# Optimization experiments

Hardware: AMD Instinct MI355X
Metric: run time of the kernel (lower is better)

Reference implementation:

```python
import jax, jax.numpy as jnp
import numpy as np

N = 100000     # total points
PBS = 500      # point_batch_size (hard-coded in module)
K = 100        # num_neighbors
KP = 15        # num_kernel_points
EPS = 1e-5


def _bn(x, g, b, axes):
    # torch BatchNorm in training mode: batch stats, biased variance
    m = jnp.mean(x, axis=axes, keepdims=True)
    v = jnp.var(x, axis=axes, keepdims=True)
    return (x - m) / jnp.sqrt(v + EPS) * g + b


def setup_inputs() -> dict:
    key = jax.random.key(0)
    ks = jax.random.split(key, 16)
    rn = lambda k, sh, s=1.0: jax.random.normal(k, sh, jnp.float32) * s
    return {
        "pts": rn(ks[0], (N, 3)),
        "normal": rn(ks[1], (N, 3)),
        "kp_points": rn(ks[2], (KP, 3)),
        "kp_weights": rn(ks[3], (KP, 3, 128), 0.3),
        "kp_sigma": jnp.float32(1.0),
        "conv1_w": rn(ks[4], (1024, 128), 128 ** -0.5),
        "conv1_b": rn(ks[5], (1024,), 0.02),
        "bn1_g": jnp.ones((1024,), jnp.float32),
        "bn1_b": jnp.zeros((1024,), jnp.float32),
        "fc1_w": rn(ks[6], (512, 1024), 1024 ** -0.5),
        "fc1_b": rn(ks[7], (512,), 0.02),
        "bn4_g": jnp.ones((512,), jnp.float32),
        "bn4_b": jnp.zeros((512,), jnp.float32),
        "fc2_w": rn(ks[8], (256, 512), 512 ** -0.5),
        "fc2_b": rn(ks[9], (256,), 0.02),
        "bn5_g": jnp.ones((256,), jnp.float32),
        "bn5_b": jnp.zeros((256,), jnp.float32),
        "fc3_w": rn(ks[10], (3, 256), 256 ** -0.5),
        "fc3_b": rn(ks[11], (3,), 0.02),
        "index": jax.random.randint(ks[12], (PBS,), 0, N, jnp.int32),
    }


def reference(pts, normal, kp_points, kp_weights, kp_sigma,
              conv1_w, conv1_b, bn1_g, bn1_b,
              fc1_w, fc1_b, bn4_g, bn4_b,
              fc2_w, fc2_b, bn5_g, bn5_b,
              fc3_w, fc3_b, index):
    sel = pts[index]                                               # [B,3]
    # L-inf pairwise distance and kNN (topk of -dist, as in the torch code)
    dist = jnp.max(jnp.abs(sel[:, None, :] - pts[None, :, :]), axis=-1)  # [B,N]
    _, nbr = jax.lax.top_k(-dist, K)                               # [B,K]
    rel = pts[nbr] - sel[:, None, :]                               # [B,K,3]

    # KPConv: gaussian weights vs kernel points, per-kernel-point linear map
    d2 = jnp.sum((rel[:, :, None, :] - kp_points[None, None]) ** 2, axis=-1)  # [B,K,KP]
    w = jnp.exp(-0.5 * d2 / (kp_sigma ** 2))
    wf = rel[:, :, None, :] * w[..., None]                         # [B,K,KP,3]
    h = jax.nn.relu(jnp.einsum('bnkc,kco->bno', wf, kp_weights))   # [B,K,128]

    # 1x1 conv 128->1024, relu then BN over (batch, points) per channel
    h = jnp.einsum('bnc,oc->bno', h, conv1_w) + conv1_b            # [B,K,1024]
    h = _bn(jax.nn.relu(h), bn1_g, bn1_b, (0, 1))
    feat = jnp.max(h, axis=1)                                      # [B,1024]

    feat = _bn(jax.nn.relu(feat @ fc1_w.T + fc1_b), bn4_g, bn4_b, (0,))
    feat = _bn(jax.nn.relu(feat @ fc2_w.T + fc2_b), bn5_g, bn5_b, (0,))
    feat = feat @ fc3_w.T + fc3_b                                  # [B,3]
    return feat, normal[index]
```

## Files before the change

### kernel.cpp

```cpp
#include <hip/hip_runtime.h>
#include <hip/hip_fp16.h>

#define NPTS 100000
#define NB 500
#define KNN 100
#define KPN 15
#define C1 128
#define C2 1024
#define C3 512
#define C4 256

typedef _Float16 half8 __attribute__((ext_vector_type(8)));
typedef float f32x4 __attribute__((ext_vector_type(4)));

__global__ __launch_bounds__(256) void gather_kernel(
    const float* __restrict__ pts, const float* __restrict__ normal,
    const int* __restrict__ index, float* __restrict__ sel,
    float* __restrict__ out2) {
  int b = blockIdx.x * 256 + threadIdx.x;
  if (b >= NB) return;
  int i = index[b];
  sel[b * 3 + 0] = pts[3 * i + 0];
  sel[b * 3 + 1] = pts[3 * i + 1];
  sel[b * 3 + 2] = pts[3 * i + 2];
  out2[b * 3 + 0] = normal[3 * i + 0];
  out2[b * 3 + 1] = normal[3 * i + 1];
  out2[b * 3 + 2] = normal[3 * i + 2];
}

#define KT 1024

__device__ __forceinline__ unsigned linf_bits(float px, float py, float pz,
                                              float sx, float sy, float sz) {
  float dx = fabsf(px - sx), dy = fabsf(py - sy), dz = fabsf(pz - sz);
  return __float_as_uint(fmaxf(fmaxf(dx, dy), dz));
}

__global__ __launch_bounds__(KT) void knn_kernel(
    const float* __restrict__ pts, const float* __restrict__ sel,
    int* __restrict__ nbr) {
  const int b = blockIdx.x;
  const int tid = threadIdx.x;
  __shared__ unsigned hist[4096];
  __shared__ unsigned chunksum[256];
  __shared__ unsigned s_prefix;
  __shared__ int s_kneed, s_base, s_cnt, s_direct, s_cnt2;
  __shared__ unsigned cand_bits[1024];
  __shared__ int cand_idx[1024];

  const float sx = sel[b * 3 + 0], sy = sel[b * 3 + 1], sz = sel[b * 3 + 2];
  const float4* base4 = (const float4*)pts;

  for (int j = tid; j < 4096; j += KT) hist[j] = 0;
  __syncthreads();
  {
    float4 c[6], n[6];
    int i0 = tid * 8;
#pragma unroll
    for (int j = 0; j < 6; ++j) c[j] = base4[(i0 * 3) / 4 + j];
    for (int it = 0; it < 12; ++it) {
      if (it + 1 < 12) {
        int i1 = (it + 1) * 8192 + tid * 8;
#pragma unroll
        for (int j = 0; j < 6; ++j) n[j] = base4[(i1 * 3) / 4 + j];
      }
      float px[8], py[8], pz[8];
      px[0] = c[0].x; py[0] = c[0].y; pz[0] = c[0].z;
      px[1] = c[0].w; py[1] = c[1].x; pz[1] = c[1].y;
      px[2] = c[1].z; py[2] = c[1].w; pz[2] = c[2].x;
      px[3] = c[2].y; py[3] = c[2].z; pz[3] = c[2].w;
      px[4] = c[3].x; py[4] = c[3].y; pz[4] = c[3].z;
      px[5] = c[3].w; py[5] = c[4].x; pz[5] = c[4].y;
      px[6] = c[4].z; py[6] = c[4].w; pz[6] = c[5].x;
      px[7] = c[5].y; py[7] = c[5].z; pz[7] = c[5].w;
#pragma unroll
      for (int j = 0; j < 8; ++j) {
        unsigned bits = linf_bits(px[j], py[j], pz[j], sx, sy, sz);
        atomicAdd(&hist[bits >> 19], 1u);
      }
#pragma unroll
      for (int j = 0; j < 6; ++j) c[j] = n[j];
    }
    for (int i = 98304 + tid; i < NPTS; i += KT) {
      unsigned bits =
          linf_bits(pts[3 * i], pts[3 * i + 1], pts[3 * i + 2], sx, sy, sz);
      atomicAdd(&hist[bits >> 19], 1u);
    }
  }

  unsigned shift = 19, prefix = 0, pendwidth = 0;
  int kneed = KNN;
  for (int pass = 0;; ++pass) {
    __syncthreads();
    if (tid < 256) {
      unsigned csum = 0;
      for (int j = 0; j < 16; ++j) csum += hist[tid * 16 + j];
      chunksum[tid] = csum;
    }
    __syncthreads();
    if (tid == 0) {
      unsigned need = (unsigned)kneed;
      unsigned cum = 0;
      int chunk = 0;
      while (chunk < 255 && cum + chunksum[chunk] < need) {
        cum += chunksum[chunk];
        ++chunk;
      }
      int bin = chunk * 16;
      while (cum + hist[bin] < need) {
        cum += hist[bin];
        ++bin;
      }
      s_kneed = (int)(need - cum);
      s_base = (int)cum;
      s_prefix = (unsigned)bin;
      s_cnt = (int)hist[bin];
    }
    __syncthreads();
    int bincnt = s_cnt;
    kneed = s_kneed;
    prefix = (pass == 0) ? s_prefix : ((prefix << pendwidth) | s_prefix);
    if (bincnt <= 1024 || shift == 0) break;
    unsigned fshift = shift;
    unsigned nshift = (shift == 19) ? 7u : 0u;
    pendwidth = (shift == 19) ? 12u : 7u;
    __syncthreads();
    for (int j = tid; j < 4096; j += KT) hist[j] = 0;
    __syncthreads();
    for (int i = tid; i < NPTS; i += KT) {
      unsigned bits =
          linf_bits(pts[3 * i], pts[3 * i + 1], pts[3 * i + 2], sx, sy, sz);
      if ((bits >> fshift) == prefix) {
        unsigned bin = (nshift == 7u) ? ((bits >> 7) & 4095u) : (bits & 127u);
        atomicAdd(&hist[bin], 1u);
      }
    }
    shift = nshift;
  }

  if (tid == 0) {
    s_direct = 0;
    s_cnt2 = 0;
  }
  __syncthreads();
  {
    float4 c[6], n[6];
    int i0 = tid * 8;
#pragma unroll
    for (int j = 0; j < 6; ++j) c[j] = base4[(i0 * 3) / 4 + j];
    for (int it = 0; it < 12; ++it) {
      if (it + 1 < 12) {
        int i1 = (it + 1) * 8192 + tid * 8;
#pragma unroll
        for (int j = 0; j < 6; ++j) n[j] = base4[(i1 * 3) / 4 + j];
      }
      float px[8], py[8], pz[8];
      px[0] = c[0].x; py[0] = c[0].y; pz[0] = c[0].z;
      px[1] = c[0].w; py[1] = c[1].x; pz[1] = c[1].y;
      px[2] = c[1].z; py[2] = c[1].w; pz[2] = c[2].x;
      px[3] = c[2].y; py[3] = c[2].z; pz[3] = c[2].w;
      px[4] = c[3].x; py[4] = c[3].y; pz[4] = c[3].z;
      px[5] = c[3].w; py[5] = c[4].x; pz[5] = c[4].y;
      px[6] = c[4].z; py[6] = c[4].w; pz[6] = c[5].x;
      px[7] = c[5].y; py[7] = c[5].z; pz[7] = c[5].w;
      int ibase = it * 8192 + tid * 8;
#pragma unroll
      for (int j = 0; j < 8; ++j) {
        unsigned bits = linf_bits(px[j], py[j], pz[j], sx, sy, sz);
        unsigned v = bits >> shift;
        if (v < prefix) {
          int pos = atomicAdd(&s_direct, 1);
          nbr[b * KNN + pos] = ibase + j;
        } else if (v == prefix) {
          int e = atomicAdd(&s_cnt2, 1);
          if (e < 1024) {
            cand_bits[e] = bits;
            cand_idx[e] = ibase + j;
          }
        }
      }
#pragma unroll
      for (int j = 0; j < 6; ++j) c[j] = n[j];
    }
    for (int i = 98304 + tid; i < NPTS; i += KT) {
      unsigned bits =
          linf_bits(pts[3 * i], pts[3 * i + 1], pts[3 * i + 2], sx, sy, sz);
      unsigned v = bits >> shift;
      if (v < prefix) {
        int pos = atomicAdd(&s_direct, 1);
        nbr[b * KNN + pos] = i;
      } else if (v == prefix) {
        int e = atomicAdd(&s_cnt2, 1);
        if (e < 1024) {
          cand_bits[e] = bits;
          cand_idx[e] = i;
        }
      }
    }
  }
  __syncthreads();

  int m = s_cnt2 < 1024 ? s_cnt2 : 1024;
  int base = s_direct;
  for (int c = tid; c < m; c += KT) {
    unsigned bc = cand_bits[c];
    int ic = cand_idx[c];
    int rank = 0;
    for (int j = 0; j < m; ++j) {
      unsigned bj = cand_bits[j];
      rank += (bj < bc || (bj == bc && cand_idx[j] < ic)) ? 1 : 0;
    }
    if (rank < kneed) nbr[b * KNN + base + rank] = ic;
  }
}

__global__ __launch_bounds__(256) void convert_kernel(
    const float* __restrict__ w1, const float* __restrict__ kpw,
    __half* __restrict__ wh, __half* __restrict__ kpwT_hi,
    __half* __restrict__ kpwT_lo) {
  int i = blockIdx.x * 256 + threadIdx.x;
  if (i < C2 * C1) wh[i] = __float2half(w1[i]);
  if (i < 128 * 64) {
    int o = i >> 6, j = i & 63;
    float v = (j < 45) ? kpw[j * 128 + o] : 0.f;
    __half hi = __float2half_rn(v);
    kpwT_hi[i] = hi;
    kpwT_lo[i] = __float2half_rn(v - __half2float(hi));
  }
}

__global__ __launch_bounds__(256) void kpconv_mfma_kernel(
    const float* __restrict__ pts, const float* __restrict__ sel,
    const int* __restrict__ nbr, const float* __restrict__ kp_points,
    const __half* __restrict__ kpwT_hi, const __half* __restrict__ kpwT_lo,
    const float* __restrict__ kp_sigma, __half* __restrict__ h) {
  const int b = blockIdx.x;
  const int tid = threadIdx.x;
  const int wave = tid >> 6, lane = tid & 63;
  const int lr = lane & 15, quad = lane >> 4;
  __shared__ __half As_hi[112 * 72];
  __shared__ __half As_lo[112 * 72];
  __shared__ __half Bs_hi[128 * 72];
  __shared__ __half Bs_lo[128 * 72];
  __shared__ float rel[100][4];
  __shared__ float kpp[48];

  for (int i = tid; i < 128 * 8; i += 256) {
    int row = i >> 3, seg = i & 7;
    *(float4*)&Bs_hi[row * 72 + seg * 8] =
        *(const float4*)&kpwT_hi[row * 64 + seg * 8];
    *(float4*)&Bs_lo[row * 72 + seg * 8] =
        *(const float4*)&kpwT_lo[row * 64 + seg * 8];
  }
  {
    float4 z = make_float4(0.f, 0.f, 0.f, 0.f);
    for (int i = tid; i < 112 * 8; i += 256) {
      int row = i >> 3, seg = i & 7;
      *(float4*)&As_hi[row * 72 + seg * 8] = z;
      *(float4*)&As_lo[row * 72 + seg * 8] = z;
    }
  }
  if (tid < 45) kpp[tid] = kp_points[tid];
  if (tid < 100) {
    int idx = nbr[b * KNN + tid];
    rel[tid][0] = pts[3 * idx + 0] - sel[b * 3 + 0];
    rel[tid][1] = pts[3 * idx + 1] - sel[b * 3 + 1];
    rel[tid][2] = pts[3 * idx + 2] - sel[b * 3 + 2];
  }
  __syncthreads();

  const float sg = kp_sigma[0];
  const float inv2s2 = -0.5f / (sg * sg);
  for (int i = tid; i < 100 * KPN; i += 256) {
    int k = i / KPN, p = i - k * KPN;
    float rx = rel[k][0] - kpp[p * 3 + 0];
    float ry = rel[k][1] - kpp[p * 3 + 1];
    float rz = rel[k][2] - kpp[p * 3 + 2];
    float w = expf(inv2s2 * (rx * rx + ry * ry + rz * rz));
#pragma unroll
    for (int c = 0; c < 3; ++c) {
      float a = rel[k][c] * w;
      __half hi = __float2half_rn(a);
      As_hi[k * 72 + p * 3 + c] = hi;
      As_lo[k * 72 + p * 3 + c] = __float2half_rn(a - __half2float(hi));
    }
  }
  __syncthreads();

  f32x4 acc[2][7];
#pragma unroll
  for (int t = 0; t < 2; ++t)
#pragma unroll
    for (int m = 0; m < 7; ++m) acc[t][m] = (f32x4)(0.f);

#pragma unroll
  for (int s = 0; s < 2; ++s) {
    half8 bhi[2], blo[2];
#pragma unroll
    for (int t = 0; t < 2; ++t) {
      int boff = ((wave * 2 + t) * 16 + lr) * 72 + s * 32 + quad * 8;
      bhi[t] = *(const half8*)&Bs_hi[boff];
      blo[t] = *(const half8*)&Bs_lo[boff];
    }
#pragma unroll
    for (int m = 0; m < 7; ++m) {
      int aoff = (m * 16 + lr) * 72 + s * 32 + quad * 8;
      half8 ahi = *(const half8*)&As_hi[aoff];
      half8 alo = *(const half8*)&As_lo[aoff];
#pragma unroll
      for (int t = 0; t < 2; ++t) {
        acc[t][m] = __builtin_amdgcn_mfma_f32_16x16x32_f16(ahi, bhi[t],
                                                           acc[t][m], 0, 0, 0);
        acc[t][m] = __builtin_amdgcn_mfma_f32_16x16x32_f16(ahi, blo[t],
                                                           acc[t][m], 0, 0, 0);
        acc[t][m] = __builtin_amdgcn_mfma_f32_16x16x32_f16(alo, bhi[t],
                                                           acc[t][m], 0, 0, 0);
      }
    }
  }

#pragma unroll
  for (int t = 0; t < 2; ++t) {
    int col = (wave * 2 + t) * 16 + lr;
#pragma unroll
    for (int m = 0; m < 7; ++m)
#pragma unroll
      for (int r = 0; r < 4; ++r) {
        int row = m * 16 + quad * 4 + r;
        if (row < 100)
          h[(b * KNN + row) * 128 + col] =
              __float2half_rn(fmaxf(acc[t][m][r], 0.f));
      }
  }
}

__global__ __launch_bounds__(256) void conv1_mfma_kernel(
    const __half* __restrict__ h16, const __half* __restrict__ wh,
    const float* __restrict__ bias, float* __restrict__ featmax,
    float* __restrict__ featmin, float* __restrict__ bnsum,
    float* __restrict__ bnsq) {
  const int b = blockIdx.y;
  const int n0 = blockIdx.x * 128;
  const int tid = threadIdx.x;
  const int wave = tid >> 6, lane = tid & 63;
  const int lr = lane & 15, quad = lane >> 4;
  __shared__ __half Hs[112 * 136];
  __shared__ __half Ws[128 * 136];

  for (int i = tid; i < 112 * 16; i += 256) {
    int row = i >> 4, seg = i & 15;
    float4 v = make_float4(0.f, 0.f, 0.f, 0.f);
    if (row < 100) v = *(const float4*)&h16[(b * 100 + row) * 128 + seg * 8];
    *(float4*)&Hs[row * 136 + seg * 8] = v;
  }
  for (int i = tid; i < 128 * 16; i += 256) {
    int row = i >> 4, seg = i & 15;
    *(float4*)&Ws[row * 136 + seg * 8] =
        *(const float4*)&wh[(n0 + row) * 128 + seg * 8];
  }
  __syncthreads();

  f32x4 acc[2][7];
#pragma unroll
  for (int t = 0; t < 2; ++t)
#pragma unroll
    for (int m = 0; m < 7; ++m) acc[t][m] = (f32x4)(0.f);

#pragma unroll
  for (int s = 0; s < 4; ++s) {
    half8 bfrag[2];
#pragma unroll
    for (int t = 0; t < 2; ++t)
      bfrag[t] =
          *(const half8*)&Ws[((wave * 2 + t) * 16 + lr) * 136 + s * 32 + quad * 8];
#pragma unroll
    for (int m = 0; m < 7; ++m) {
      half8 afrag = *(const half8*)&Hs[(m * 16 + lr) * 136 + s * 32 + quad * 8];
      acc[0][m] =
          __builtin_amdgcn_mfma_f32_16x16x32_f16(afrag, bfrag[0], acc[0][m], 0, 0, 0);
      acc[1][m] =
          __builtin_amdgcn_mfma_f32_16x16x32_f16(afrag, bfrag[1], acc[1][m], 0, 0, 0);
    }
  }

#pragma unroll
  for (int t = 0; t < 2; ++t) {
    int col = n0 + (wave * 2 + t) * 16 + lr;
    float bv = bias[col];
    float pmax = -1e30f, pmin = 1e30f, psum = 0.f, psq = 0.f;
#pragma unroll
    for (int m = 0; m < 7; ++m)
#pragma unroll
      for (int r = 0; r < 4; ++r) {
        int row = m * 16 + quad * 4 + r;
        if (row < 100) {
          float y = fmaxf(acc[t][m][r] + bv, 0.f);
          pmax = fmaxf(pmax, y);
          pmin = fminf(pmin, y);
          psum += y;
          psq += y * y;
        }
      }
    pmax = fmaxf(pmax, __shfl_xor(pmax, 16));
    pmax = fmaxf(pmax, __shfl_xor(pmax, 32));
    pmin = fminf(pmin, __shfl_xor(pmin, 16));
    pmin = fminf(pmin, __shfl_xor(pmin, 32));
    psum += __shfl_xor(psum, 16);
    psum += __shfl_xor(psum, 32);
    psq += __shfl_xor(psq, 16);
    psq += __shfl_xor(psq, 32);
    if (quad == 0) {
      featmax[b * C2 + col] = pmax;
      featmin[b * C2 + col] = pmin;
      atomicAdd(&bnsum[col], psum);
      atomicAdd(&bnsq[col], psq);
    }
  }
}

__global__ __launch_bounds__(256) void bn1max_kernel(
    const float* __restrict__ featmax, const float* __restrict__ featmin,
    const float* __restrict__ bnsum, const float* __restrict__ bnsq,
    const float* __restrict__ g, const float* __restrict__ bb,
    float* __restrict__ feat1) {
  int idx = blockIdx.x * 256 + threadIdx.x;
  if (idx >= NB * C2) return;
  int o = idx & (C2 - 1);
  const float invn = 1.f / (float)(NB * KNN);
  float m = bnsum[o] * invn;
  float v = bnsq[o] * invn - m * m;
  float a = g[o] / sqrtf(v + 1e-5f);
  float x = (a >= 0.f) ? featmax[idx] : featmin[idx];
  feat1[idx] = (x - m) * a + bb[o];
}

template <int KDIM>
__global__ __launch_bounds__(256) void fc_relu_stats_kernel(
    const float* __restrict__ x,
    const float* __restrict__ w,
    const float* __restrict__ bias, float* __restrict__ yraw,
    float* __restrict__ s, float* __restrict__ sq, int ncols) {
  const int r0 = blockIdx.x * 4;
  const int n0 = blockIdx.y * 64;
  const int tid = threadIdx.x;
  const int col = tid >> 2;
  const int row = tid & 3;
  __shared__ float xs[4][1028];
  __shared__ float ws[64][132];
  for (int f = tid; f < KDIM; f += 256) {
    int rr = f / (KDIM / 4), kq = (f % (KDIM / 4)) * 4;
    *(float4*)&xs[rr][kq] = *(const float4*)&x[(r0 + rr) * KDIM + kq];
  }
  float acc = 0.f;
  for (int kc = 0; kc < KDIM; kc += 128) {
    __syncthreads();
#pragma unroll
    for (int i = 0; i < 8; ++i) {
      int f = tid + i * 256;
      int cr = f >> 5, kq = (f & 31) * 4;
      *(float4*)&ws[cr][kq] = *(const float4*)&w[(n0 + cr) * KDIM + kc + kq];
    }
    __syncthreads();
    for (int kk = 0; kk < 128; kk += 4) {
      float4 xv = *(float4*)&xs[row][kc + kk];
      float4 wv = *(float4*)&ws[col][kk];
      acc += xv.x * wv.x + xv.y * wv.y + xv.z * wv.z + xv.w * wv.w;
    }
  }
  float y = fmaxf(acc + bias[n0 + col], 0.f);
  yraw[(r0 + row) * ncols + n0 + col] = y;
  float ys = y, y2 = y * y;
  ys += __shfl_xor(ys, 1); y2 += __shfl_xor(y2, 1);
  ys += __shfl_xor(ys, 2); y2 += __shfl_xor(y2, 2);
  if (row == 0) {
    atomicAdd(&s[n0 + col], ys);
    atomicAdd(&sq[n0 + col], y2);
  }
}

__global__ __launch_bounds__(256) void bn_finalize_kernel(
    const float* __restrict__ yraw, const float* __restrict__ s,
    const float* __restrict__ sq, const float* __restrict__ g,
    const float* __restrict__ bb, float* __restrict__ out, int ncols) {
  int idx = blockIdx.x * 256 + threadIdx.x;
  if (idx >= NB * ncols) return;
  int o = idx & (ncols - 1);
  float m = s[o] * (1.f / (float)NB);
  float v = sq[o] * (1.f / (float)NB) - m * m;
  float a = g[o] / sqrtf(v + 1e-5f);
  out[idx] = (yraw[idx] - m) * a + bb[o];
}

__global__ __launch_bounds__(256) void fc3_kernel(
    const float* __restrict__ feat, const float* __restrict__ w,
    const float* __restrict__ bias, float* __restrict__ out) {
  int idx = blockIdx.x * 256 + threadIdx.x;
  if (idx >= NB * 3) return;
  int b = idx / 3, o = idx % 3;
  float acc = 0.f;
  for (int k = 0; k < C4; ++k) acc += feat[b * C4 + k] * w[o * C4 + k];
  out[idx] = acc + bias[o];
}

extern "C" void kernel_launch(void* const* d_in, const int* in_sizes, int n_in,
                              void* d_out, int out_size, void* d_ws,
                              size_t ws_size, hipStream_t stream) {
  const float* pts = (const float*)d_in[0];
  const float* normal = (const float*)d_in[1];
  const float* kp_points = (const float*)d_in[2];
  const float* kp_weights = (const float*)d_in[3];
  const float* kp_sigma = (const float*)d_in[4];
  const float* conv1_w = (const float*)d_in[5];
  const float* conv1_b = (const float*)d_in[6];
  const float* bn1_g = (const float*)d_in[7];
  const float* bn1_b = (const float*)d_in[8];
  const float* fc1_w = (const float*)d_in[9];
  const float* fc1_b = (const float*)d_in[10];
  const float* bn4_g = (const float*)d_in[11];
  const float* bn4_b = (const float*)d_in[12];
  const float* fc2_w = (const float*)d_in[13];
  const float* fc2_b = (const float*)d_in[14];
  const float* bn5_g = (const float*)d_in[15];
  const float* bn5_b = (const float*)d_in[16];
  const float* fc3_w = (const float*)d_in[17];
  const float* fc3_b = (const float*)d_in[18];
  const int* index = (const int*)d_in[19];
  float* out = (float*)d_out;

  char* p = (char*)d_ws;
  auto carve = [&](size_t bytes) {
    void* r = (void*)p;
    p += (bytes + 255) & ~(size_t)255;
    return r;
  };
  float* sel = (float*)carve(NB * 3 * 4);
  int* nbr = (int*)carve(NB * KNN * 4);
  __half* h = (__half*)carve((size_t)NB * KNN * C1 * 2);
  __half* wh = (__half*)carve((size_t)C2 * C1 * 2);
  __half* kpwT_hi = (__half*)carve((size_t)128 * 64 * 2);
  __half* kpwT_lo = (__half*)carve((size_t)128 * 64 * 2);
  float* featmax = (float*)carve(NB * C2 * 4);
  float* featmin = (float*)carve(NB * C2 * 4);
  float* feat1 = (float*)carve(NB * C2 * 4);
  float* f2raw = (float*)carve(NB * C3 * 4);
  float* feat2 = (float*)carve(NB * C3 * 4);
  float* f3raw = (float*)carve(NB * C4 * 4);
  float* feat3 = (float*)carve(NB * C4 * 4);
  float* stats = (float*)carve((2 * C2 + 2 * C3 + 2 * C4) * 4);
  float* bnsum = stats;
  float* bnsq = stats + C2;
  float* s4 = stats + 2 * C2;
  float* sq4 = s4 + C3;
  float* s5 = sq4 + C3;
  float* sq5 = s5 + C4;

  hipMemsetAsync(stats, 0, (2 * C2 + 2 * C3 + 2 * C4) * 4, stream);

  gather_kernel<<<2, 256, 0, stream>>>(pts, normal, index, sel, out + NB * 3);
  knn_kernel<<<NB, KT, 0, stream>>>(pts, sel, nbr);
  convert_kernel<<<(C2 * C1 + 255) / 256, 256, 0, stream>>>(
      conv1_w, kp_weights, wh, kpwT_hi, kpwT_lo);
  kpconv_mfma_kernel<<<NB, 256, 0, stream>>>(pts, sel, nbr, kp_points, kpwT_hi,
                                             kpwT_lo, kp_sigma, h);
  conv1_mfma_kernel<<<dim3(8, NB), 256, 0, stream>>>(h, wh, conv1_b, featmax,
                                                     featmin, bnsum, bnsq);
  bn1max_kernel<<<(NB * C2 + 255) / 256, 256, 0, stream>>>(
      featmax, featmin, bnsum, bnsq, bn1_g, bn1_b, feat1);
  fc_relu_stats_kernel<C2><<<dim3(125, C3 / 64), 256, 0, stream>>>(
      feat1, fc1_w, fc1_b, f2raw, s4, sq4, C3);
  bn_finalize_kernel<<<(NB * C3 + 255) / 256, 256, 0, stream>>>(
      f2raw, s4, sq4, bn4_g, bn4_b, feat2, C3);
  fc_relu_stats_kernel<C3><<<dim3(125, C4 / 64), 256, 0, stream>>>(
      feat2, fc2_w, fc2_b, f3raw, s5, sq5, C4);
  bn_finalize_kernel<<<(NB * C4 + 255) / 256, 256, 0, stream>>>(
      f3raw, s5, sq5, bn5_g, bn5_b, feat3, C4);
  fc3_kernel<<<(NB * 3 + 255) / 256, 256, 0, stream>>>(feat3, fc3_w, fc3_b,
                                                       out);
}
```

Measured before the change: 285.8 us.

## Process two queries per kNN block and fold BatchNorm into downstream FC kernels

The kNN kernel now handles two query points per 1024-thread block, so every streamed point is loaded once and used for two L-inf distance histograms and the candidate selection. This halves the global reads of the point cloud. The first histogram uses 2048 bins per query instead of 4096, and the candidate cap drops to 768, which changes how often refinement passes are needed. Separately, the gather kernel is folded into the kNN and convert kernels, and the BN-apply kernels are fused into the loads of the following FC kernels and fc3, removing several launches and intermediate buffers.

```diff
diff --git a/kernel.cpp b/kernel.cpp
--- a/kernel.cpp
+++ b/kernel.cpp
@@ -13,22 +13,11 @@
 typedef _Float16 half8 __attribute__((ext_vector_type(8)));
 typedef float f32x4 __attribute__((ext_vector_type(4)));
 
-__global__ __launch_bounds__(256) void gather_kernel(
-    const float* __restrict__ pts, const float* __restrict__ normal,
-    const int* __restrict__ index, float* __restrict__ sel,
-    float* __restrict__ out2) {
-  int b = blockIdx.x * 256 + threadIdx.x;
-  if (b >= NB) return;
-  int i = index[b];
-  sel[b * 3 + 0] = pts[3 * i + 0];
-  sel[b * 3 + 1] = pts[3 * i + 1];
-  sel[b * 3 + 2] = pts[3 * i + 2];
-  out2[b * 3 + 0] = normal[3 * i + 0];
-  out2[b * 3 + 1] = normal[3 * i + 1];
-  out2[b * 3 + 2] = normal[3 * i + 2];
-}
-
+#define QB 2
 #define KT 1024
+#define CAP 768
+#define HS 20
+#define HBINS 2048
 
 __device__ __forceinline__ unsigned linf_bits(float px, float py, float pz,
                                               float sx, float sy, float sz) {
@@ -37,187 +26,215 @@
 }
 
 __global__ __launch_bounds__(KT) void knn_kernel(
-    const float* __restrict__ pts, const float* __restrict__ sel,
-    int* __restrict__ nbr) {
+    const float* __restrict__ pts, const int* __restrict__ index,
+    float* __restrict__ sel, int* __restrict__ nbr) {
   const int b = blockIdx.x;
   const int tid = threadIdx.x;
-  __shared__ unsigned hist[4096];
-  __shared__ unsigned chunksum[256];
-  __shared__ unsigned s_prefix;
-  __shared__ int s_kneed, s_base, s_cnt, s_direct, s_cnt2;
-  __shared__ unsigned cand_bits[1024];
-  __shared__ int cand_idx[1024];
-
-  const float sx = sel[b * 3 + 0], sy = sel[b * 3 + 1], sz = sel[b * 3 + 2];
+  __shared__ unsigned hist[QB * HBINS];
+  __shared__ unsigned chunk[QB][256];
+  __shared__ float qs[QB][3];
+  __shared__ int s_kneed[QB], s_cnt[QB], s_shift[QB];
+  __shared__ unsigned s_prefix[QB];
+  __shared__ int s_direct[QB], s_cnt2[QB];
+  __shared__ unsigned cand_bits[QB][CAP];
+  __shared__ int cand_idx[QB][CAP];
+
+  for (int j = tid; j < QB * HBINS; j += KT) hist[j] = 0;
+  if (tid < QB * 3) {
+    int q = tid / 3, c = tid % 3;
+    float v = pts[3 * index[b * QB + q] + c];
+    qs[q][c] = v;
+    sel[(b * QB + q) * 3 + c] = v;
+  }
+  __syncthreads();
+  const float sx0 = qs[0][0], sy0 = qs[0][1], sz0 = qs[0][2];
+  const float sx1 = qs[1][0], sy1 = qs[1][1], sz1 = qs[1][2];
   const float4* base4 = (const float4*)pts;
 
-  for (int j = tid; j < 4096; j += KT) hist[j] = 0;
-  __syncthreads();
   {
-    float4 c[6], n[6];
+    float4 c6[6], n6[6];
     int i0 = tid * 8;
 #pragma unroll
-    for (int j = 0; j < 6; ++j) c[j] = base4[(i0 * 3) / 4 + j];
+    for (int j = 0; j < 6; ++j) c6[j] = base4[(i0 * 3) / 4 + j];
     for (int it = 0; it < 12; ++it) {
       if (it + 1 < 12) {
         int i1 = (it + 1) * 8192 + tid * 8;
 #pragma unroll
-        for (int j = 0; j < 6; ++j) n[j] = base4[(i1 * 3) / 4 + j];
+        for (int j = 0; j < 6; ++j) n6[j] = base4[(i1 * 3) / 4 + j];
       }
       float px[8], py[8], pz[8];
-      px[0] = c[0].x; py[0] = c[0].y; pz[0] = c[0].z;
-      px[1] = c[0].w; py[1] = c[1].x; pz[1] = c[1].y;
-      px[2] = c[1].z; py[2] = c[1].w; pz[2] = c[2].x;
-      px[3] = c[2].y; py[3] = c[2].z; pz[3] = c[2].w;
-      px[4] = c[3].x; py[4] = c[3].y; pz[4] = c[3].z;
-      px[5] = c[3].w; py[5] = c[4].x; pz[5] = c[4].y;
-      px[6] = c[4].z; py[6] = c[4].w; pz[6] = c[5].x;
-      px[7] = c[5].y; py[7] = c[5].z; pz[7] = c[5].w;
+      px[0] = c6[0].x; py[0] = c6[0].y; pz[0] = c6[0].z;
+      px[1] = c6[0].w; py[1] = c6[1].x; pz[1] = c6[1].y;
+      px[2] = c6[1].z; py[2] = c6[1].w; pz[2] = c6[2].x;
+      px[3] = c6[2].y; py[3] = c6[2].z; pz[3] = c6[2].w;
+      px[4] = c6[3].x; py[4] = c6[3].y; pz[4] = c6[3].z;
+      px[5] = c6[3].w; py[5] = c6[4].x; pz[5] = c6[4].y;
+      px[6] = c6[4].z; py[6] = c6[4].w; pz[6] = c6[5].x;
+      px[7] = c6[5].y; py[7] = c6[5].z; pz[7] = c6[5].w;
 #pragma unroll
       for (int j = 0; j < 8; ++j) {
-        unsigned bits = linf_bits(px[j], py[j], pz[j], sx, sy, sz);
-        atomicAdd(&hist[bits >> 19], 1u);
-      }
-#pragma unroll
-      for (int j = 0; j < 6; ++j) c[j] = n[j];
+        unsigned b0 = linf_bits(px[j], py[j], pz[j], sx0, sy0, sz0);
+        unsigned b1 = linf_bits(px[j], py[j], pz[j], sx1, sy1, sz1);
+        atomicAdd(&hist[b0 >> HS], 1u);
+        atomicAdd(&hist[HBINS + (b1 >> HS)], 1u);
+      }
+#pragma unroll
+      for (int j = 0; j < 6; ++j) c6[j] = n6[j];
     }
     for (int i = 98304 + tid; i < NPTS; i += KT) {
-      unsigned bits =
-          linf_bits(pts[3 * i], pts[3 * i + 1], pts[3 * i + 2], sx, sy, sz);
-      atomicAdd(&hist[bits >> 19], 1u);
-    }
-  }
-
-  unsigned shift = 19, prefix = 0, pendwidth = 0;
-  int kneed = KNN;
-  for (int pass = 0;; ++pass) {
-    __syncthreads();
-    if (tid < 256) {
-      unsigned csum = 0;
-      for (int j = 0; j < 16; ++j) csum += hist[tid * 16 + j];
-      chunksum[tid] = csum;
-    }
-    __syncthreads();
-    if (tid == 0) {
-      unsigned need = (unsigned)kneed;
-      unsigned cum = 0;
-      int chunk = 0;
-      while (chunk < 255 && cum + chunksum[chunk] < need) {
-        cum += chunksum[chunk];
-        ++chunk;
-      }
-      int bin = chunk * 16;
-      while (cum + hist[bin] < need) {
-        cum += hist[bin];
-        ++bin;
-      }
-      s_kneed = (int)(need - cum);
-      s_base = (int)cum;
-      s_prefix = (unsigned)bin;
-      s_cnt = (int)hist[bin];
-    }
-    __syncthreads();
-    int bincnt = s_cnt;
-    kneed = s_kneed;
-    prefix = (pass == 0) ? s_prefix : ((prefix << pendwidth) | s_prefix);
-    if (bincnt <= 1024 || shift == 0) break;
-    unsigned fshift = shift;
-    unsigned nshift = (shift == 19) ? 7u : 0u;
-    pendwidth = (shift == 19) ? 12u : 7u;
-    __syncthreads();
-    for (int j = tid; j < 4096; j += KT) hist[j] = 0;
-    __syncthreads();
-    for (int i = tid; i < NPTS; i += KT) {
-      unsigned bits =
-          linf_bits(pts[3 * i], pts[3 * i + 1], pts[3 * i + 2], sx, sy, sz);
-      if ((bits >> fshift) == prefix) {
-        unsigned bin = (nshift == 7u) ? ((bits >> 7) & 4095u) : (bits & 127u);
-        atomicAdd(&hist[bin], 1u);
-      }
-    }
-    shift = nshift;
-  }
-
-  if (tid == 0) {
-    s_direct = 0;
-    s_cnt2 = 0;
-  }
-  __syncthreads();
+      float px = pts[3 * i], py = pts[3 * i + 1], pz = pts[3 * i + 2];
+      atomicAdd(&hist[linf_bits(px, py, pz, sx0, sy0, sz0) >> HS], 1u);
+      atomicAdd(&hist[HBINS + (linf_bits(px, py, pz, sx1, sy1, sz1) >> HS)], 1u);
+    }
+  }
+  __syncthreads();
+
+  if (tid < QB * 256) {
+    int q = tid >> 8, c = tid & 255;
+    unsigned s = 0;
+    for (int j = 0; j < 8; ++j) s += hist[q * HBINS + c * 8 + j];
+    chunk[q][c] = s;
+  }
+  __syncthreads();
+  if (tid < QB) {
+    int q = tid;
+    unsigned need = KNN, cum = 0;
+    int ch = 0;
+    while (ch < 255 && cum + chunk[q][ch] < need) { cum += chunk[q][ch]; ++ch; }
+    int bin = ch * 8;
+    while (cum + hist[q * HBINS + bin] < need) {
+      cum += hist[q * HBINS + bin];
+      ++bin;
+    }
+    s_kneed[q] = (int)(need - cum);
+    s_prefix[q] = (unsigned)bin;
+    s_cnt[q] = (int)hist[q * HBINS + bin];
+    s_shift[q] = HS;
+    s_direct[q] = 0;
+    s_cnt2[q] = 0;
+  }
+
+  for (int q = 0; q < QB; ++q) {
+    for (;;) {
+      __syncthreads();
+      if (s_cnt[q] <= CAP || s_shift[q] == 0) break;
+      const int fsh = s_shift[q];
+      const unsigned pfx = s_prefix[q];
+      const int nsh = (fsh == HS) ? 8 : 0;
+      const int nb = (fsh == HS) ? 4096 : 256;
+      const float qx = qs[q][0], qy = qs[q][1], qz = qs[q][2];
+      for (int j = tid; j < nb; j += KT) hist[j] = 0;
+      __syncthreads();
+      for (int i = tid; i < NPTS; i += KT) {
+        unsigned bits =
+            linf_bits(pts[3 * i], pts[3 * i + 1], pts[3 * i + 2], qx, qy, qz);
+        if ((bits >> fsh) == pfx) atomicAdd(&hist[(bits >> nsh) & (nb - 1)], 1u);
+      }
+      __syncthreads();
+      if (tid == 0) {
+        unsigned need = (unsigned)s_kneed[q], cum = 0;
+        int bin = 0;
+        while (cum + hist[bin] < need) { cum += hist[bin]; ++bin; }
+        s_kneed[q] = (int)(need - cum);
+        s_cnt[q] = (int)hist[bin];
+        s_prefix[q] = (pfx << ((fsh == HS) ? 12 : 8)) | (unsigned)bin;
+        s_shift[q] = nsh;
+      }
+    }
+  }
+  __syncthreads();
+  const int sh0 = s_shift[0], sh1 = s_shift[1];
+  const unsigned pf0 = s_prefix[0], pf1 = s_prefix[1];
+
   {
-    float4 c[6], n[6];
+    float4 c6[6], n6[6];
     int i0 = tid * 8;
 #pragma unroll
-    for (int j = 0; j < 6; ++j) c[j] = base4[(i0 * 3) / 4 + j];
+    for (int j = 0; j < 6; ++j) c6[j] = base4[(i0 * 3) / 4 + j];
     for (int it = 0; it < 12; ++it) {
       if (it + 1 < 12) {
         int i1 = (it + 1) * 8192 + tid * 8;
 #pragma unroll
-        for (int j = 0; j < 6; ++j) n[j] = base4[(i1 * 3) / 4 + j];
+        for (int j = 0; j < 6; ++j) n6[j] = base4[(i1 * 3) / 4 + j];
       }
       float px[8], py[8], pz[8];
-      px[0] = c[0].x; py[0] = c[0].y; pz[0] = c[0].z;
-      px[1] = c[0].w; py[1] = c[1].x; pz[1] = c[1].y;
-      px[2] = c[1].z; py[2] = c[1].w; pz[2] = c[2].x;
-      px[3] = c[2].y; py[3] = c[2].z; pz[3] = c[2].w;
-      px[4] = c[3].x; py[4] = c[3].y; pz[4] = c[3].z;
-      px[5] = c[3].w; py[5] = c[4].x; pz[5] = c[4].y;
-      px[6] = c[4].z; py[6] = c[4].w; pz[6] = c[5].x;
-      px[7] = c[5].y; py[7] = c[5].z; pz[7] = c[5].w;
+      px[0] = c6[0].x; py[0] = c6[0].y; pz[0] = c6[0].z;
+      px[1] = c6[0].w; py[1] = c6[1].x; pz[1] = c6[1].y;
+      px[2] = c6[1].z; py[2] = c6[1].w; pz[2] = c6[2].x;
+      px[3] = c6[2].y; py[3] = c6[2].z; pz[3] = c6[2].w;
+      px[4] = c6[3].x; py[4] = c6[3].y; pz[4] = c6[3].z;
+      px[5] = c6[3].w; py[5] = c6[4].x; pz[5] = c6[4].y;
+      px[6] = c6[4].z; py[6] = c6[4].w; pz[6] = c6[5].x;
+      px[7] = c6[5].y; py[7] = c6[5].z; pz[7] = c6[5].w;
       int ibase = it * 8192 + tid * 8;
 #pragma unroll
       for (int j = 0; j < 8; ++j) {
-        unsigned bits = linf_bits(px[j], py[j], pz[j], sx, sy, sz);
-        unsigned v = bits >> shift;
-        if (v < prefix) {
-          int pos = atomicAdd(&s_direct, 1);
-          nbr[b * KNN + pos] = ibase + j;
-        } else if (v == prefix) {
-          int e = atomicAdd(&s_cnt2, 1);
-          if (e < 1024) {
-            cand_bits[e] = bits;
-            cand_idx[e] = ibase + j;
-          }
+        unsigned b0 = linf_bits(px[j], py[j], pz[j], sx0, sy0, sz0);
+        unsigned b1 = linf_bits(px[j], py[j], pz[j], sx1, sy1, sz1);
+        unsigned v0 = b0 >> sh0, v1 = b1 >> sh1;
+        if (v0 < pf0) {
+          int pos = atomicAdd(&s_direct[0], 1);
+          nbr[(b * QB + 0) * KNN + pos] = ibase + j;
+        } else if (v0 == pf0) {
+          int e = atomicAdd(&s_cnt2[0], 1);
+          if (e < CAP) { cand_bits[0][e] = b0; cand_idx[0][e] = ibase + j; }
         }
-      }
-#pragma unroll
-      for (int j = 0; j < 6; ++j) c[j] = n[j];
+        if (v1 < pf1) {
+          int pos = atomicAdd(&s_direct[1], 1);
+          nbr[(b * QB + 1) * KNN + pos] = ibase + j;
+        } else if (v1 == pf1) {
+          int e = atomicAdd(&s_cnt2[1], 1);
+          if (e < CAP) { cand_bits[1][e] = b1; cand_idx[1][e] = ibase + j; }
+        }
+      }
+#pragma unroll
+      for (int j = 0; j < 6; ++j) c6[j] = n6[j];
     }
     for (int i = 98304 + tid; i < NPTS; i += KT) {
-      unsigned bits =
-          linf_bits(pts[3 * i], pts[3 * i + 1], pts[3 * i + 2], sx, sy, sz);
-      unsigned v = bits >> shift;
-      if (v < prefix) {
-        int pos = atomicAdd(&s_direct, 1);
-        nbr[b * KNN + pos] = i;
-      } else if (v == prefix) {
-        int e = atomicAdd(&s_cnt2, 1);
-        if (e < 1024) {
-          cand_bits[e] = bits;
-          cand_idx[e] = i;
-        }
-      }
-    }
-  }
-  __syncthreads();
-
-  int m = s_cnt2 < 1024 ? s_cnt2 : 1024;
-  int base = s_direct;
-  for (int c = tid; c < m; c += KT) {
-    unsigned bc = cand_bits[c];
-    int ic = cand_idx[c];
-    int rank = 0;
-    for (int j = 0; j < m; ++j) {
-      unsigned bj = cand_bits[j];
-      rank += (bj < bc || (bj == bc && cand_idx[j] < ic)) ? 1 : 0;
-    }
-    if (rank < kneed) nbr[b * KNN + base + rank] = ic;
+      float px = pts[3 * i], py = pts[3 * i + 1], pz = pts[3 * i + 2];
+      unsigned b0 = linf_bits(px, py, pz, sx0, sy0, sz0);
+      unsigned b1 = linf_bits(px, py, pz, sx1, sy1, sz1);
+      unsigned v0 = b0 >> sh0, v1 = b1 >> sh1;
+      if (v0 < pf0) {
+        int pos = atomicAdd(&s_direct[0], 1);
+        nbr[(b * QB + 0) * KNN + pos] = i;
+      } else if (v0 == pf0) {
+        int e = atomicAdd(&s_cnt2[0], 1);
+        if (e < CAP) { cand_bits[0][e] = b0; cand_idx[0][e] = i; }
+      }
+      if (v1 < pf1) {
+        int pos = atomicAdd(&s_direct[1], 1);
+        nbr[(b * QB + 1) * KNN + pos] = i;
+      } else if (v1 == pf1) {
+        int e = atomicAdd(&s_cnt2[1], 1);
+        if (e < CAP) { cand_bits[1][e] = b1; cand_idx[1][e] = i; }
+      }
+    }
+  }
+  __syncthreads();
+
+  for (int q = 0; q < QB; ++q) {
+    int m = s_cnt2[q] < CAP ? s_cnt2[q] : CAP;
+    int base = s_direct[q];
+    int kneedq = s_kneed[q];
+    for (int c = tid; c < m; c += KT) {
+      unsigned bc = cand_bits[q][c];
+      int ic = cand_idx[q][c];
+      int rank = 0;
+      for (int j = 0; j < m; ++j) {
+        unsigned bj = cand_bits[q][j];
+        rank += (bj < bc || (bj == bc && cand_idx[q][j] < ic)) ? 1 : 0;
+      }
+      if (rank < kneedq) nbr[(b * QB + q) * KNN + base + rank] = ic;
+    }
   }
 }
 
 __global__ __launch_bounds__(256) void convert_kernel(
     const float* __restrict__ w1, const float* __restrict__ kpw,
+    const float* __restrict__ normal, const int* __restrict__ index,
     __half* __restrict__ wh, __half* __restrict__ kpwT_hi,
-    __half* __restrict__ kpwT_lo) {
+    __half* __restrict__ kpwT_lo, float* __restrict__ out2) {
   int i = blockIdx.x * 256 + threadIdx.x;
   if (i < C2 * C1) wh[i] = __float2half(w1[i]);
   if (i < 128 * 64) {
@@ -226,6 +243,10 @@
     __half hi = __float2half_rn(v);
     kpwT_hi[i] = hi;
     kpwT_lo[i] = __float2half_rn(v - __half2float(hi));
+  }
+  if (i < NB * 3) {
+    int b = i / 3, c = i % 3;
+    out2[i] = normal[3 * index[b] + c];
   }
 }
 
@@ -418,38 +439,49 @@
   }
 }
 
-__global__ __launch_bounds__(256) void bn1max_kernel(
-    const float* __restrict__ featmax, const float* __restrict__ featmin,
-    const float* __restrict__ bnsum, const float* __restrict__ bnsq,
-    const float* __restrict__ g, const float* __restrict__ bb,
-    float* __restrict__ feat1) {
-  int idx = blockIdx.x * 256 + threadIdx.x;
-  if (idx >= NB * C2) return;
-  int o = idx & (C2 - 1);
-  const float invn = 1.f / (float)(NB * KNN);
-  float m = bnsum[o] * invn;
-  float v = bnsq[o] * invn - m * m;
-  float a = g[o] / sqrtf(v + 1e-5f);
-  float x = (a >= 0.f) ? featmax[idx] : featmin[idx];
-  feat1[idx] = (x - m) * a + bb[o];
-}
-
-template <int KDIM>
-__global__ __launch_bounds__(256) void fc_relu_stats_kernel(
-    const float* __restrict__ x,
-    const float* __restrict__ w,
-    const float* __restrict__ bias, float* __restrict__ yraw,
-    float* __restrict__ s, float* __restrict__ sq, int ncols) {
+template <int KDIM, int MODE>
+__global__ __launch_bounds__(256) void fc_bn_relu_stats_kernel(
+    const float* __restrict__ x1, const float* __restrict__ x2,
+    const float* __restrict__ sstat, const float* __restrict__ sqstat,
+    const float* __restrict__ bng, const float* __restrict__ bnb,
+    const float* __restrict__ w, const float* __restrict__ bias,
+    float* __restrict__ yraw, float* __restrict__ s, float* __restrict__ sq,
+    int ncols) {
   const int r0 = blockIdx.x * 4;
   const int n0 = blockIdx.y * 64;
   const int tid = threadIdx.x;
   const int col = tid >> 2;
   const int row = tid & 3;
-  __shared__ float xs[4][1028];
+  __shared__ float xs[4][KDIM + 4];
   __shared__ float ws[64][132];
+  __shared__ float ao[KDIM], off[KDIM];
+  const float invn = (MODE == 1) ? (1.f / (float)(NB * KNN)) : (1.f / (float)NB);
+  for (int k = tid; k < KDIM; k += 256) {
+    float m = sstat[k] * invn;
+    float v = sqstat[k] * invn - m * m;
+    float a = bng[k] / sqrtf(v + 1e-5f);
+    ao[k] = a;
+    off[k] = bnb[k] - m * a;
+  }
+  __syncthreads();
   for (int f = tid; f < KDIM; f += 256) {
     int rr = f / (KDIM / 4), kq = (f % (KDIM / 4)) * 4;
-    *(float4*)&xs[rr][kq] = *(const float4*)&x[(r0 + rr) * KDIM + kq];
+    float4 xm = *(const float4*)&x1[(r0 + rr) * KDIM + kq];
+    float v1[4] = {xm.x, xm.y, xm.z, xm.w};
+    if constexpr (MODE == 1) {
+      float4 xn = *(const float4*)&x2[(r0 + rr) * KDIM + kq];
+      float v2[4] = {xn.x, xn.y, xn.z, xn.w};
+#pragma unroll
+      for (int j = 0; j < 4; ++j) {
+        float a = ao[kq + j];
+        float x = (a >= 0.f) ? v1[j] : v2[j];
+        xs[rr][kq + j] = x * a + off[kq + j];
+      }
+    } else {
+#pragma unroll
+      for (int j = 0; j < 4; ++j)
+        xs[rr][kq + j] = v1[j] * ao[kq + j] + off[kq + j];
+    }
   }
   float acc = 0.f;
   for (int kc = 0; kc < KDIM; kc += 128) {
@@ -478,27 +510,27 @@
   }
 }
 
-__global__ __launch_bounds__(256) void bn_finalize_kernel(
-    const float* __restrict__ yraw, const float* __restrict__ s,
-    const float* __restrict__ sq, const float* __restrict__ g,
-    const float* __restrict__ bb, float* __restrict__ out, int ncols) {
-  int idx = blockIdx.x * 256 + threadIdx.x;
-  if (idx >= NB * ncols) return;
-  int o = idx & (ncols - 1);
-  float m = s[o] * (1.f / (float)NB);
-  float v = sq[o] * (1.f / (float)NB) - m * m;
-  float a = g[o] / sqrtf(v + 1e-5f);
-  out[idx] = (yraw[idx] - m) * a + bb[o];
-}
-
-__global__ __launch_bounds__(256) void fc3_kernel(
-    const float* __restrict__ feat, const float* __restrict__ w,
+__global__ __launch_bounds__(256) void fc3_bn_kernel(
+    const float* __restrict__ f3raw, const float* __restrict__ s5,
+    const float* __restrict__ sq5, const float* __restrict__ g5,
+    const float* __restrict__ b5, const float* __restrict__ w,
     const float* __restrict__ bias, float* __restrict__ out) {
-  int idx = blockIdx.x * 256 + threadIdx.x;
+  __shared__ float ao[C4], off[C4];
+  int tid = threadIdx.x;
+  {
+    float m = s5[tid] * (1.f / (float)NB);
+    float v = sq5[tid] * (1.f / (float)NB) - m * m;
+    float a = g5[tid] / sqrtf(v + 1e-5f);
+    ao[tid] = a;
+    off[tid] = b5[tid] - m * a;
+  }
+  __syncthreads();
+  int idx = blockIdx.x * 256 + tid;
   if (idx >= NB * 3) return;
   int b = idx / 3, o = idx % 3;
   float acc = 0.f;
-  for (int k = 0; k < C4; ++k) acc += feat[b * C4 + k] * w[o * C4 + k];
+  for (int k = 0; k < C4; ++k)
+    acc += (f3raw[b * C4 + k] * ao[k] + off[k]) * w[o * C4 + k];
   out[idx] = acc + bias[o];
 }
 
@@ -541,11 +573,8 @@
   __half* kpwT_lo = (__half*)carve((size_t)128 * 64 * 2);
   float* featmax = (float*)carve(NB * C2 * 4);
   float* featmin = (float*)carve(NB * C2 * 4);
-  float* feat1 = (float*)carve(NB * C2 * 4);
   float* f2raw = (float*)carve(NB * C3 * 4);
-  float* feat2 = (float*)carve(NB * C3 * 4);
   float* f3raw = (float*)carve(NB * C4 * 4);
-  float* feat3 = (float*)carve(NB * C4 * 4);
   float* stats = (float*)carve((2 * C2 + 2 * C3 + 2 * C4) * 4);
   float* bnsum = stats;
   float* bnsq = stats + C2;
@@ -556,24 +585,18 @@
 
   hipMemsetAsync(stats, 0, (2 * C2 + 2 * C3 + 2 * C4) * 4, stream);
 
-  gather_kernel<<<2, 256, 0, stream>>>(pts, normal, index, sel, out + NB * 3);
-  knn_kernel<<<NB, KT, 0, stream>>>(pts, sel, nbr);
+  knn_kernel<<<NB / QB, KT, 0, stream>>>(pts, index, sel, nbr);
   convert_kernel<<<(C2 * C1 + 255) / 256, 256, 0, stream>>>(
-      conv1_w, kp_weights, wh, kpwT_hi, kpwT_lo);
+      conv1_w, kp_weights, normal, index, wh, kpwT_hi, kpwT_lo, out + NB * 3);
   kpconv_mfma_kernel<<<NB, 256, 0, stream>>>(pts, sel, nbr, kp_points, kpwT_hi,
                                              kpwT_lo, kp_sigma, h);
   conv1_mfma_kernel<<<dim3(8, NB), 256, 0, stream>>>(h, wh, conv1_b, featmax,
                                                      featmin, bnsum, bnsq);
-  bn1max_kernel<<<(NB * C2 + 255) / 256, 256, 0, stream>>>(
-      featmax, featmin, bnsum, bnsq, bn1_g, bn1_b, feat1);
-  fc_relu_stats_kernel<C2><<<dim3(125, C3 / 64), 256, 0, stream>>>(
-      feat1, fc1_w, fc1_b, f2raw, s4, sq4, C3);
-  bn_finalize_kernel<<<(NB * C3 + 255) / 256, 256, 0, stream>>>(
-      f2raw, s4, sq4, bn4_g, bn4_b, feat2, C3);
-  fc_relu_stats_kernel<C3><<<dim3(125, C4 / 64), 256, 0, stream>>>(
-      feat2, fc2_w, fc2_b, f3raw, s5, sq5, C4);
-  bn_finalize_kernel<<<(NB * C4 + 255) / 256, 256, 0, stream>>>(
-      f3raw, s5, sq5, bn5_g, bn5_b, feat3, C4);
-  fc3_kernel<<<(NB * 3 + 255) / 256, 256, 0, stream>>>(feat3, fc3_w, fc3_b,
-                                                       out);
-}
+  fc_bn_relu_stats_kernel<C2, 1><<<dim3(125, C3 / 64), 256, 0, stream>>>(
+      featmax, featmin, bnsum, bnsq, bn1_g, bn1_b, fc1_w, fc1_b, f2raw, s4,
+      sq4, C3);
+  fc_bn_relu_stats_kernel<C3, 2><<<dim3(125, C4 / 64), 256, 0, stream>>>(
+      f2raw, nullptr, s4, sq4, bn4_g, bn4_b, fc2_w, fc2_b, f3raw, s5, sq5, C4);
+  fc3_bn_kernel<<<(NB * 3 + 255) / 256, 256, 0, stream>>>(
+      f3raw, s5, sq5, bn5_g, bn5_b, fc3_w, fc3_b, out);
+}
```

Measured after the change: 317.3 us. 1.11x slower.
